# Optimization experiments

Hardware: AMD Instinct MI355X
Metric: run time of the kernel (lower is better)

## Reference

```python
import jax, jax.numpy as jnp
import numpy as np


def _layer_norm(x, g, b, eps=1e-5):
    mu = x.mean(-1, keepdims=True)
    var = ((x - mu) ** 2).mean(-1, keepdims=True)
    return (x - mu) * jax.lax.rsqrt(var + eps) * g + b


def _linear(x, w, b):
    # torch nn.Linear: y = x @ W^T + b, w has shape (out, in)
    return jnp.einsum('...i,oi->...o', x, w) + b


def setup_inputs() -> dict:
    key = jax.random.key(0)
    ks = jax.random.split(key, 12)
    B, N, C = 1, 512, 128
    s = 0.02  # weight init scale
    f32 = jnp.float32
    return {
        'X': jax.random.normal(ks[0], (B, N, N, C), f32),
        'mask': jax.random.randint(ks[1], (B, N, N, 1), 0, 2) > 0,
        # first LayerNorm
        'ln1_g': jnp.ones((C,), f32), 'ln1_b': jnp.zeros((C,), f32),
        # left edge MLP: Linear -> Sigmoid -> Linear
        'lw1': jax.random.normal(ks[2], (C, C), f32) * s, 'lb1': jnp.zeros((C,), f32),
        'lw2': jax.random.normal(ks[3], (C, C), f32) * s, 'lb2': jnp.zeros((C,), f32),
        # right edge MLP
        'rw1': jax.random.normal(ks[4], (C, C), f32) * s, 'rb1': jnp.zeros((C,), f32),
        'rw2': jax.random.normal(ks[5], (C, C), f32) * s, 'rb2': jnp.zeros((C,), f32),
        # skip gate: Linear -> Sigmoid
        'sw': jax.random.normal(ks[6], (C, C), f32) * s, 'sb': jnp.zeros((C,), f32),
        # combine: LayerNorm -> Linear
        'ln2_g': jnp.ones((C,), f32), 'ln2_b': jnp.zeros((C,), f32),
        'cw': jax.random.normal(ks[7], (C, C), f32) * s, 'cb': jnp.zeros((C,), f32),
    }


def reference(X, mask, ln1_g, ln1_b, lw1, lb1, lw2, lb2,
              rw1, rb1, rw2, rb2, sw, sb, ln2_g, ln2_b, cw, cb):
    h = _layer_norm(X, ln1_g, ln1_b)                      # (B,N,N,C)
    A = _linear(jax.nn.sigmoid(_linear(h, lw1, lb1)), lw2, lb2)
    Bm = _linear(jax.nn.sigmoid(_linear(h, rw1, rb1)), rw2, rb2)
    G = jax.nn.sigmoid(_linear(h, sw, sb))
    A = jnp.where(mask, A, 0.0)
    Bm = jnp.where(mask, Bm, 0.0)
    # triangle multiplication, 'outgoing': contract over k per channel
    T = jnp.einsum('bikc,bjkc->bijc', A, Bm)              # (B,N,N,C)
    Y = _linear(_layer_norm(T, ln2_g, ln2_b), cw, cb) * G
    return Y
```

## Files before the change

kernel.cpp:

```cpp
#include <hip/hip_runtime.h>

typedef unsigned short u16;
typedef unsigned int   u32;
typedef u32   u32x4  __attribute__((ext_vector_type(4)));
typedef __bf16 bf16x8 __attribute__((ext_vector_type(8)));
typedef float f32x4  __attribute__((ext_vector_type(4)));

#define NPOS (512*512)
#define WSLOT 16384

__device__ __forceinline__ u16 f2bf(float f){
  __bf16 h=(__bf16)f;
  return __builtin_bit_cast(u16,h);
}
__device__ __forceinline__ float bf2f(u16 s){ u32 u=((u32)s)<<16; return __builtin_bit_cast(float,u); }
union pk8 { u16 s[8]; u32x4 v; };

__device__ __forceinline__ void gload16(const void* g, void* l){
  __builtin_amdgcn_global_load_lds((const __attribute__((address_space(1))) void*)g,
                                   (__attribute__((address_space(3))) void*)l, 16, 0, 0);
}

__device__ __forceinline__ bf16x8 cvt8(const float* p){
  f32x4 w0=*(const f32x4*)p, w1=*(const f32x4*)(p+4);
  bf16x8 b;
#pragma unroll
  for(int e=0;e<4;e++){ b[e]=(__bf16)w0[e]; b[4+e]=(__bf16)w1[e]; }
  return b;
}

__global__ __launch_bounds__(256) void k0(
    const float* __restrict__ lw1, const float* __restrict__ lw2,
    const float* __restrict__ rw1, const float* __restrict__ rw2,
    const float* __restrict__ sw,  const float* __restrict__ cw, u16* __restrict__ Wp)
{
  const float* srcs[6]={lw1,lw2,rw1,rw2,sw,cw};
  const float* W=srcs[blockIdx.x];
  u16* dst=Wp + (size_t)blockIdx.x*WSLOT;
  const int t=threadIdx.x, lane=t&63, wvv=t>>6, lr=lane&15, quad=lane>>4;
#pragma unroll
  for(int i=0;i<8;i++){
    int tile=wvv*8+i, nt=tile>>2, kk=tile&3;
    const float* p=W+(size_t)(nt*16+lr)*128+kk*32+quad*8;
    bf16x8 b=cvt8(p);
    *(u32x4*)(dst+((size_t)tile*64+lane)*8)=__builtin_bit_cast(u32x4,b);
  }
}

__device__ __forceinline__ void wave_gemm2(const u16 (*sh)[136], int wv, int lane,
    const u16* __restrict__ Wp, const float* __restrict__ bias, float o[4][2][4])
{
  const int lr=lane&15, quad=lane>>4;
  bf16x8 b[2][4];
#pragma unroll
  for(int n2=0;n2<2;n2++){
    const int nt=wv*2+n2;
#pragma unroll
    for(int kk=0;kk<4;kk++)
      b[n2][kk]=*(const bf16x8*)(Wp+((size_t)((nt*4+kk)*64+lane))*8);
  }
  float bv[2]={bias[(wv*2)*16+lr], bias[(wv*2+1)*16+lr]};
#pragma unroll
  for(int mt=0;mt<4;mt++){
    bf16x8 a[4];
#pragma unroll
    for(int kk=0;kk<4;kk++) a[kk]=*(const bf16x8*)&sh[mt*16+lr][kk*32+quad*8];
#pragma unroll
    for(int n2=0;n2<2;n2++){
      f32x4 acc={0.f,0.f,0.f,0.f};
#pragma unroll
      for(int kk=0;kk<4;kk++)
        acc=__builtin_amdgcn_mfma_f32_16x16x32_bf16(a[kk],b[n2][kk],acc,0,0,0);
#pragma unroll
      for(int r=0;r<4;r++) o[mt][n2][r]=acc[r]+bv[n2];
    }
  }
}

__device__ __forceinline__ void sig_to_lds2(u16 (*sh)[136], int wv,int lane, float o[4][2][4]){
  const int lr=lane&15, quad=lane>>4;
#pragma unroll
  for(int mt=0;mt<4;mt++)
#pragma unroll
    for(int n2=0;n2<2;n2++)
#pragma unroll
      for(int r=0;r<4;r++)
        sh[mt*16+quad*4+r][(wv*2+n2)*16+lr]=f2bf(1.f/(1.f+__expf(-o[mt][n2][r])));
}

__device__ __forceinline__ void mask_to_lds2(u16 (*sh)[136], int wv,int lane, float o[4][2][4], const float* smask){
  const int lr=lane&15, quad=lane>>4;
#pragma unroll
  for(int mt=0;mt<4;mt++)
#pragma unroll
    for(int n2=0;n2<2;n2++)
#pragma unroll
      for(int r=0;r<4;r++){
        int row=mt*16+quad*4+r;
        sh[row][(wv*2+n2)*16+lr]=f2bf(o[mt][n2][r]*smask[row]);
      }
}

__device__ __forceinline__ void store_tr(const u16 (*sh)[136], int t, u16* __restrict__ dst, int p0){
#pragma unroll
  for(int iter=0;iter<4;iter++){
    int c=iter*32+(t>>3);
    int pos=(t&7)*8;
    pk8 u;
#pragma unroll
    for(int r=0;r<8;r++){
      int rp=(r+(t>>3)+(t&7))&7;
      u.s[rp]=sh[pos+rp][c];
    }
    *(u32x4*)(dst+(size_t)c*NPOS+p0+pos)=u.v;
  }
}

__global__ __launch_bounds__(256,3) void k1(
    const float* __restrict__ X, const void* __restrict__ mask,
    const float* __restrict__ g1, const float* __restrict__ b1,
    const u16* __restrict__ Wp,
    const float* __restrict__ lb1, const float* __restrict__ lb2,
    const float* __restrict__ rb1, const float* __restrict__ rb2,
    const float* __restrict__ sb,
    u16* __restrict__ At, u16* __restrict__ Bt, float* __restrict__ G)
{
  __shared__ u16 shh [64][136];
  __shared__ u16 shtL[64][136];
  __shared__ u16 shtR[64][136];
  __shared__ float smask[64];
  __shared__ int mpacked;
  const int t=threadIdx.x;
  const int p0=blockIdx.x*64;
  if(t==0){
    const int* m32=(const int*)mask;
    int pk=0;
#pragma unroll
    for(int i=0;i<32;i++){ u32 v=(u32)m32[i]; if(v>1u) pk=1; }
    mpacked=pk;
  }
  {
    int row=t>>2, q=t&3;
    const float* xp = X + (size_t)(p0+row)*128 + q*32;
    float v[32]; float s=0.f,s2=0.f;
#pragma unroll
    for(int u=0;u<8;u++){ f32x4 d=*(const f32x4*)(xp+u*4);
#pragma unroll
      for(int e=0;e<4;e++) v[u*4+e]=d[e]; }
#pragma unroll
    for(int i=0;i<32;i++){ s+=v[i]; s2+=v[i]*v[i]; }
    s+=__shfl_xor(s,1); s2+=__shfl_xor(s2,1);
    s+=__shfl_xor(s,2); s2+=__shfl_xor(s2,2);
    float mu=s*(1.f/128.f);
    float rstd=1.f/sqrtf(s2*(1.f/128.f)-mu*mu+1e-5f);
#pragma unroll
    for(int u=0;u<4;u++){
      pk8 o;
#pragma unroll
      for(int e=0;e<8;e++){
        int c=q*32+u*8+e;
        o.s[e]=f2bf((v[u*8+e]-mu)*rstd*g1[c]+b1[c]);
      }
      *(u32x4*)&shh[row][q*32+u*8]=o.v;
    }
  }
  __syncthreads();
  if(t<64){
    int p=p0+t;
    int mval = mpacked ? (int)((const unsigned char*)mask)[p] : ((const int*)mask)[p];
    smask[t]=(mval!=0)?1.f:0.f;
  }
  const int lane=t&63, wv=t>>6;
  float oL[4][2][4], oR[4][2][4];
  wave_gemm2(shh,wv,lane,Wp+0*WSLOT,lb1,oL);
  wave_gemm2(shh,wv,lane,Wp+2*WSLOT,rb1,oR);
  sig_to_lds2(shtL,wv,lane,oL);
  sig_to_lds2(shtR,wv,lane,oR);
  __syncthreads();
  wave_gemm2(shtL,wv,lane,Wp+1*WSLOT,lb2,oL);
  wave_gemm2(shtR,wv,lane,Wp+3*WSLOT,rb2,oR);
  __syncthreads();
  mask_to_lds2(shtL,wv,lane,oL,smask);
  mask_to_lds2(shtR,wv,lane,oR,smask);
  __syncthreads();
  store_tr(shtL,t,At,p0);
  store_tr(shtR,t,Bt,p0);
  wave_gemm2(shh,wv,lane,Wp+4*WSLOT,sb,oL);
  const int lr=lane&15, quad=lane>>4;
#pragma unroll
  for(int mt=0;mt<4;mt++)
#pragma unroll
    for(int n2=0;n2<2;n2++)
#pragma unroll
      for(int r=0;r<4;r++){
        size_t p=p0+mt*16+quad*4+r;
        G[p*128+(wv*2+n2)*16+lr]=1.f/(1.f+__expf(-oL[mt][n2][r]));
      }
}

__global__ __launch_bounds__(256) void k2(const u16* __restrict__ At, const u16* __restrict__ Bt,
                                          u16* __restrict__ T, int j_base, int jc)
{
  __shared__ u16 sA[128*64];
  __shared__ u16 sB[128*64];
  const int t=threadIdx.x, lane=t&63, wv=t>>6;
  const int c=blockIdx.z;
  const int i0=blockIdx.y*128;
  const int j0l=blockIdx.x*128;
  const int wm=(wv>>1)*64, wn=(wv&1)*64, lr=lane&15, quad=lane>>4;
  const u16* Ab = At + (size_t)c*NPOS + (size_t)i0*512;
  const u16* Bb = Bt + (size_t)c*NPOS + (size_t)(j_base+j0l)*512;
  const int srow = lane>>3;
  const int scol = ((lane&7) ^ srow)*8;
  const int swz  = (lr&7)<<4;
  f32x4 acc[4][4];
#pragma unroll
  for(int i=0;i<4;i++)
#pragma unroll
    for(int j=0;j<4;j++) acc[i][j]=(f32x4){0.f,0.f,0.f,0.f};
  for(int k0=0;k0<512;k0+=64){
#pragma unroll
    for(int j=0;j<4;j++){
      int seg=wv*4+j;
      int row=seg*8+srow;
      gload16(Ab + (size_t)row*512 + k0 + scol, &sA[seg*512]);
      gload16(Bb + (size_t)row*512 + k0 + scol, &sB[seg*512]);
    }
    __syncthreads();
    const char* sAc=(const char*)sA;
    const char* sBc=(const char*)sB;
#pragma unroll
    for(int ks=0;ks<2;ks++){
      bf16x8 a[4],b[4];
#pragma unroll
      for(int mt=0;mt<4;mt++){
        int row=wm+mt*16+lr;
        a[mt]=*(const bf16x8*)(sAc + row*128 + ((ks*64+quad*16)^swz));
      }
#pragma unroll
      for(int nt=0;nt<4;nt++){
        int row=wn+nt*16+lr;
        b[nt]=*(const bf16x8*)(sBc + row*128 + ((ks*64+quad*16)^swz));
      }
#pragma unroll
      for(int mt=0;mt<4;mt++)
#pragma unroll
        for(int nt=0;nt<4;nt++)
          acc[mt][nt]=__builtin_amdgcn_mfma_f32_16x16x32_bf16(a[mt],b[nt],acc[mt][nt],0,0,0);
    }
    __syncthreads();
  }
  u16* Tb = T + (size_t)c*512*jc;
#pragma unroll
  for(int mt=0;mt<4;mt++)
#pragma unroll
    for(int nt=0;nt<4;nt++)
#pragma unroll
      for(int r=0;r<4;r++){
        int row=i0+wm+mt*16+quad*4+r;
        int col=j0l+wn+nt*16+lr;
        Tb[(size_t)row*jc+col]=f2bf(acc[mt][nt][r]);
      }
}

__global__ __launch_bounds__(256) void k3(const u16* __restrict__ T,
    const u16* __restrict__ cwp,
    const float* __restrict__ g2, const float* __restrict__ b2,
    const float* __restrict__ cb, float* GY,
    int j_base, int jc, int jshift)
{
  __shared__ u16 sH[128][136];
  const int t=threadIdx.x;
  const int cp0=blockIdx.x*128;
  {
    int c=t>>1, half=t&1;
    const u16* Tp = T + (size_t)c*512*jc + cp0 + half*64;
#pragma unroll
    for(int u=0;u<8;u++){
      pk8 d; d.v=*(const u32x4*)(Tp+u*8);
#pragma unroll
      for(int e=0;e<8;e++) sH[half*64+u*8+e][c]=d.s[e];
    }
  }
  __syncthreads();
  {
    int pos=t>>1, half=t&1;
    float v[64]; float s=0.f,s2=0.f;
#pragma unroll
    for(int u=0;u<8;u++)
#pragma unroll
      for(int e=0;e<8;e++){ float x=bf2f(sH[pos][half*64+u*8+e]); v[u*8+e]=x; s+=x; s2+=x*x; }
    s+=__shfl_xor(s,1); s2+=__shfl_xor(s2,1);
    float mu=s*(1.f/128.f);
    float rstd=1.f/sqrtf(s2*(1.f/128.f)-mu*mu+1e-5f);
#pragma unroll
    for(int u=0;u<8;u++){
      pk8 o;
#pragma unroll
      for(int e=0;e<8;e++){
        int c=half*64+u*8+e;
        o.s[e]=f2bf((v[u*8+e]-mu)*rstd*g2[c]+b2[c]);
      }
      *(u32x4*)&sH[pos][half*64+u*8]=o.v;
    }
  }
  __syncthreads();
  const int lane=t&63, wv=t>>6, m0=wv*32, lr=lane&15, quad=lane>>4;
  bf16x8 a[2][4];
#pragma unroll
  for(int mt=0;mt<2;mt++)
#pragma unroll
    for(int kk=0;kk<4;kk++) a[mt][kk]=*(const bf16x8*)&sH[m0+mt*16+lr][kk*32+quad*8];
#pragma unroll
  for(int nt=0;nt<8;nt++){
    f32x4 a0={0.f,0.f,0.f,0.f}, a1={0.f,0.f,0.f,0.f};
#pragma unroll
    for(int kk=0;kk<4;kk++){
      bf16x8 b=*(const bf16x8*)(cwp+((size_t)((nt*4+kk)*64+lane))*8);
      a0=__builtin_amdgcn_mfma_f32_16x16x32_bf16(a[0][kk],b,a0,0,0,0);
      a1=__builtin_amdgcn_mfma_f32_16x16x32_bf16(a[1][kk],b,a1,0,0,0);
    }
    float cbv=cb[nt*16+lr];
#pragma unroll
    for(int mt=0;mt<2;mt++){
      f32x4 ac = mt? a1: a0;
#pragma unroll
      for(int r=0;r<4;r++){
        int l=m0+mt*16+quad*4+r;
        int pl=cp0+l;
        size_t p=((size_t)(pl>>jshift)<<9)+(size_t)j_base+(pl&(jc-1));
        int col=nt*16+lr;
        float gg=GY[p*128+col];
        GY[p*128+col]=(ac[r]+cbv)*gg;
      }
    }
  }
}

__global__ void kprobe(float* out, u32 wsmib){
  if(threadIdx.x==0 && blockIdx.x==0) out[0]=(float)wsmib;
}

extern "C" void kernel_launch(void* const* d_in, const int* in_sizes, int n_in,
                              void* d_out, int out_size, void* d_ws, size_t ws_size,
                              hipStream_t stream)
{
  (void)in_sizes; (void)n_in; (void)out_size;
  const float* X  =(const float*)d_in[0];
  const void*  mask=d_in[1];
  const float* g1 =(const float*)d_in[2];  const float* b1 =(const float*)d_in[3];
  const float* lw1=(const float*)d_in[4];  const float* lb1=(const float*)d_in[5];
  const float* lw2=(const float*)d_in[6];  const float* lb2=(const float*)d_in[7];
  const float* rw1=(const float*)d_in[8];  const float* rb1=(const float*)d_in[9];
  const float* rw2=(const float*)d_in[10]; const float* rb2=(const float*)d_in[11];
  const float* sw =(const float*)d_in[12]; const float* sb =(const float*)d_in[13];
  const float* g2 =(const float*)d_in[14]; const float* b2 =(const float*)d_in[15];
  const float* cw =(const float*)d_in[16]; const float* cb =(const float*)d_in[17];
  float* out=(float*)d_out;

  const size_t wbytes = (size_t)6*WSLOT*sizeof(u16);
  const size_t base = wbytes + 2*(size_t)NPOS*128*sizeof(u16);
  int jc=0, jshift=0;
  if      (ws_size >= base + (size_t)512*512*128*2){ jc=512; jshift=9; }
  else if (ws_size >= base + (size_t)512*256*128*2){ jc=256; jshift=8; }
  else if (ws_size >= base + (size_t)512*128*128*2){ jc=128; jshift=7; }
  if(jc==0){
    kprobe<<<dim3(1),dim3(64),0,stream>>>(out,(u32)(ws_size>>20));
    return;
  }
  u16* Wp=(u16*)d_ws;
  u16* At=Wp+(size_t)6*WSLOT;
  u16* Bt=At+(size_t)NPOS*128;
  u16* T =Bt+(size_t)NPOS*128;

  k0<<<dim3(6),dim3(256),0,stream>>>(lw1,lw2,rw1,rw2,sw,cw,Wp);
  k1<<<dim3(4096),dim3(256),0,stream>>>(X,mask,g1,b1,Wp,lb1,lb2,rb1,rb2,sb,At,Bt,out);
  for(int jb=0;jb<512;jb+=jc){
    k2<<<dim3(jc/128,4,128),dim3(256),0,stream>>>(At,Bt,T,jb,jc);
    k3<<<dim3(4*jc),dim3(256),0,stream>>>(T,Wp+(size_t)5*WSLOT,g2,b2,cb,out,jb,jc,jshift);
  }
}
```

Baseline: 548.1 us.

## Shrink k1 LDS footprint, reorder gemms, and remap k2 blocks per XCD

k1 now uses one shared staging tile instead of two: the left and right branches take turns, and the h tile is reused once it is no longer needed. The gate GEMM and G store move to the start of the kernel. The mask is applied as a 16-bit AND during the transposed store, and launch bounds are raised to four blocks per CU. k2 switches to a 1D grid whose block index is decoded so that all tiles of a channel land on the same XCD, aiming at better L2 reuse of the A/B channel planes. The costs are more barriers in k1 and possible register pressure from the higher occupancy target.

```diff
diff --git a/kernel.cpp b/kernel.cpp
--- a/kernel.cpp
+++ b/kernel.cpp
@@ -88,20 +88,19 @@
         sh[mt*16+quad*4+r][(wv*2+n2)*16+lr]=f2bf(1.f/(1.f+__expf(-o[mt][n2][r])));
 }
 
-__device__ __forceinline__ void mask_to_lds2(u16 (*sh)[136], int wv,int lane, float o[4][2][4], const float* smask){
+__device__ __forceinline__ void out_to_lds2(u16 (*sh)[136], int wv,int lane, float o[4][2][4]){
   const int lr=lane&15, quad=lane>>4;
 #pragma unroll
   for(int mt=0;mt<4;mt++)
 #pragma unroll
     for(int n2=0;n2<2;n2++)
 #pragma unroll
-      for(int r=0;r<4;r++){
-        int row=mt*16+quad*4+r;
-        sh[row][(wv*2+n2)*16+lr]=f2bf(o[mt][n2][r]*smask[row]);
-      }
-}
-
-__device__ __forceinline__ void store_tr(const u16 (*sh)[136], int t, u16* __restrict__ dst, int p0){
+      for(int r=0;r<4;r++)
+        sh[mt*16+quad*4+r][(wv*2+n2)*16+lr]=f2bf(o[mt][n2][r]);
+}
+
+__device__ __forceinline__ void store_tr_m(const u16 (*sh)[136], int t, u16* __restrict__ dst,
+                                           int p0, const u16* __restrict__ smask){
 #pragma unroll
   for(int iter=0;iter<4;iter++){
     int c=iter*32+(t>>3);
@@ -110,13 +109,13 @@
 #pragma unroll
     for(int r=0;r<8;r++){
       int rp=(r+(t>>3)+(t&7))&7;
-      u.s[rp]=sh[pos+rp][c];
+      u.s[rp]=sh[pos+rp][c] & smask[pos+rp];
     }
     *(u32x4*)(dst+(size_t)c*NPOS+p0+pos)=u.v;
   }
 }
 
-__global__ __launch_bounds__(256,3) void k1(
+__global__ __launch_bounds__(256,4) void k1(
     const float* __restrict__ X, const void* __restrict__ mask,
     const float* __restrict__ g1, const float* __restrict__ b1,
     const u16* __restrict__ Wp,
@@ -125,10 +124,9 @@
     const float* __restrict__ sb,
     u16* __restrict__ At, u16* __restrict__ Bt, float* __restrict__ G)
 {
-  __shared__ u16 shh [64][136];
-  __shared__ u16 shtL[64][136];
-  __shared__ u16 shtR[64][136];
-  __shared__ float smask[64];
+  __shared__ u16 shh[64][136];
+  __shared__ u16 sht[64][136];
+  __shared__ u16 smask16[64];
   __shared__ int mpacked;
   const int t=threadIdx.x;
   const int p0=blockIdx.x*64;
@@ -168,45 +166,52 @@
   if(t<64){
     int p=p0+t;
     int mval = mpacked ? (int)((const unsigned char*)mask)[p] : ((const int*)mask)[p];
-    smask[t]=(mval!=0)?1.f:0.f;
-  }
-  const int lane=t&63, wv=t>>6;
+    smask16[t]=(mval!=0)?(u16)0xFFFFu:(u16)0u;
+  }
+  const int lane=t&63, wv=t>>6, lr=lane&15, quad=lane>>4;
   float oL[4][2][4], oR[4][2][4];
+  {
+    float oG[4][2][4];
+    wave_gemm2(shh,wv,lane,Wp+4*WSLOT,sb,oG);
+#pragma unroll
+    for(int mt=0;mt<4;mt++)
+#pragma unroll
+      for(int n2=0;n2<2;n2++)
+#pragma unroll
+        for(int r=0;r<4;r++){
+          size_t p=p0+mt*16+quad*4+r;
+          G[p*128+(wv*2+n2)*16+lr]=1.f/(1.f+__expf(-oG[mt][n2][r]));
+        }
+  }
   wave_gemm2(shh,wv,lane,Wp+0*WSLOT,lb1,oL);
+  sig_to_lds2(sht,wv,lane,oL);
   wave_gemm2(shh,wv,lane,Wp+2*WSLOT,rb1,oR);
-  sig_to_lds2(shtL,wv,lane,oL);
-  sig_to_lds2(shtR,wv,lane,oR);
-  __syncthreads();
-  wave_gemm2(shtL,wv,lane,Wp+1*WSLOT,lb2,oL);
-  wave_gemm2(shtR,wv,lane,Wp+3*WSLOT,rb2,oR);
-  __syncthreads();
-  mask_to_lds2(shtL,wv,lane,oL,smask);
-  mask_to_lds2(shtR,wv,lane,oR,smask);
-  __syncthreads();
-  store_tr(shtL,t,At,p0);
-  store_tr(shtR,t,Bt,p0);
-  wave_gemm2(shh,wv,lane,Wp+4*WSLOT,sb,oL);
-  const int lr=lane&15, quad=lane>>4;
-#pragma unroll
-  for(int mt=0;mt<4;mt++)
-#pragma unroll
-    for(int n2=0;n2<2;n2++)
-#pragma unroll
-      for(int r=0;r<4;r++){
-        size_t p=p0+mt*16+quad*4+r;
-        G[p*128+(wv*2+n2)*16+lr]=1.f/(1.f+__expf(-oL[mt][n2][r]));
-      }
+  __syncthreads();
+  sig_to_lds2(shh,wv,lane,oR);
+  wave_gemm2(sht,wv,lane,Wp+1*WSLOT,lb2,oL);
+  __syncthreads();
+  out_to_lds2(sht,wv,lane,oL);
+  wave_gemm2(shh,wv,lane,Wp+3*WSLOT,rb2,oR);
+  __syncthreads();
+  store_tr_m(sht,t,At,p0,smask16);
+  out_to_lds2(shh,wv,lane,oR);
+  __syncthreads();
+  store_tr_m(shh,t,Bt,p0,smask16);
 }
 
 __global__ __launch_bounds__(256) void k2(const u16* __restrict__ At, const u16* __restrict__ Bt,
-                                          u16* __restrict__ T, int j_base, int jc)
+                                          u16* __restrict__ T, int j_base, int jc, int nxsh)
 {
   __shared__ u16 sA[128*64];
   __shared__ u16 sB[128*64];
   const int t=threadIdx.x, lane=t&63, wv=t>>6;
-  const int c=blockIdx.z;
-  const int i0=blockIdx.y*128;
-  const int j0l=blockIdx.x*128;
+  const int bid=blockIdx.x;
+  const int tpcsh=2+nxsh;
+  const int xcd=bid&7, q=bid>>3;
+  const int c   = xcd*16 + (q>>tpcsh);
+  const int tile= q & ((1<<tpcsh)-1);
+  const int j0l = (tile & ((1<<nxsh)-1))*128;
+  const int i0  = (tile >> nxsh)*128;
   const int wm=(wv>>1)*64, wn=(wv&1)*64, lr=lane&15, quad=lane>>4;
   const u16* Ab = At + (size_t)c*NPOS + (size_t)i0*512;
   const u16* Bb = Bt + (size_t)c*NPOS + (size_t)(j_base+j0l)*512;
@@ -360,10 +365,10 @@
 
   const size_t wbytes = (size_t)6*WSLOT*sizeof(u16);
   const size_t base = wbytes + 2*(size_t)NPOS*128*sizeof(u16);
-  int jc=0, jshift=0;
-  if      (ws_size >= base + (size_t)512*512*128*2){ jc=512; jshift=9; }
-  else if (ws_size >= base + (size_t)512*256*128*2){ jc=256; jshift=8; }
-  else if (ws_size >= base + (size_t)512*128*128*2){ jc=128; jshift=7; }
+  int jc=0, jshift=0, nxsh=0;
+  if      (ws_size >= base + (size_t)512*512*128*2){ jc=512; jshift=9; nxsh=2; }
+  else if (ws_size >= base + (size_t)512*256*128*2){ jc=256; jshift=8; nxsh=1; }
+  else if (ws_size >= base + (size_t)512*128*128*2){ jc=128; jshift=7; nxsh=0; }
   if(jc==0){
     kprobe<<<dim3(1),dim3(64),0,stream>>>(out,(u32)(ws_size>>20));
     return;
@@ -375,8 +380,9 @@
 
   k0<<<dim3(6),dim3(256),0,stream>>>(lw1,lw2,rw1,rw2,sw,cw,Wp);
   k1<<<dim3(4096),dim3(256),0,stream>>>(X,mask,g1,b1,Wp,lb1,lb2,rb1,rb2,sb,At,Bt,out);
+  const int nbl=(jc/128)*4*128;
   for(int jb=0;jb<512;jb+=jc){
-    k2<<<dim3(jc/128,4,128),dim3(256),0,stream>>>(At,Bt,T,jb,jc);
+    k2<<<dim3(nbl),dim3(256),0,stream>>>(At,Bt,T,jb,jc,nxsh);
     k3<<<dim3(4*jc),dim3(256),0,stream>>>(T,Wp+(size_t)5*WSLOT,g2,b2,cb,out,jb,jc,jshift);
   }
 }
```

Result: no change. 555.0 us (+1.3%).
